# Performance work log

Hardware: AMD Instinct MI355X
Metric: run time of the kernel (lower is better)

Reference implementation:

```python
import jax, jax.numpy as jnp
import numpy as np

NEG = jnp.float32(-1e30)  # log-semiring 'zero' (avoid -inf for safe grads)


def _ctc_total_scores(log_probs, targets, input_lengths, target_lengths):
    """Log-semiring forward over the composed CTC topology.

    log_probs: (T, N, C) log-softmax outputs, blank id = 0
    targets:   (N*L,) flat labels in [1, C)
    Returns tot_scores (N,): log p(targets | log_probs) per utterance,
    identical to k2.intersect_dense + get_tot_scores(log_semiring=True).
    """
    T, N, C = log_probs.shape
    L = targets.shape[0] // N
    tgt = targets.reshape(N, L).astype(jnp.int32)
    S = 2 * L + 1  # extended sequence: blank y1 blank y2 ... yL blank

    ext = jnp.zeros((N, S), jnp.int32).at[:, 1::2].set(tgt)
    s_idx = jnp.arange(S)
    # skip transition s-2 -> s allowed only for label states with ext[s] != ext[s-2]
    diff = jnp.concatenate([jnp.zeros((N, 2), bool), ext[:, 2:] != ext[:, :-2]], axis=1)
    skip_ok = (s_idx[None, :] % 2 == 1) & (s_idx[None, :] >= 2) & diff
    # states beyond this utterance's extended length are invalid
    valid = s_idx[None, :] <= 2 * target_lengths.astype(jnp.int32)[:, None]
    s_end = 2 * target_lengths.astype(jnp.int32)  # index of final blank state

    def emit(lp):  # (N, C) -> (N, S): gather log-probs of extended labels
        return jnp.take_along_axis(lp, ext, axis=1)

    e0 = emit(log_probs[0])
    a0 = jnp.full((N, S), NEG).at[:, 0].set(e0[:, 0]).at[:, 1].set(e0[:, 1])
    a0 = jnp.where(valid, a0, NEG)

    def final_score(a):  # logsumexp over the two accepting states
        last = jnp.take_along_axis(a, s_end[:, None], axis=1)[:, 0]
        prev = jnp.take_along_axis(a, (s_end - 1)[:, None], axis=1)[:, 0]
        return jnp.logaddexp(last, prev)

    def step(a, lp):
        sh1 = jnp.concatenate([jnp.full((N, 1), NEG), a[:, :-1]], axis=1)
        sh2 = jnp.concatenate([jnp.full((N, 2), NEG), a[:, :-2]], axis=1)
        sh2 = jnp.where(skip_ok, sh2, NEG)
        a_new = jnp.logaddexp(jnp.logaddexp(a, sh1), sh2) + emit(lp)
        a_new = jnp.where(valid, a_new, NEG)
        return a_new, final_score(a_new)

    _, finals = jax.lax.scan(step, a0, log_probs[1:])  # finals: (T-1, N)
    finals = jnp.concatenate([final_score(a0)[None], finals], axis=0)  # (T, N)
    tot = jnp.take_along_axis(finals, (input_lengths.astype(jnp.int32) - 1)[None, :], axis=0)[0]
    return tot


def setup_inputs() -> dict:
    key = jax.random.key(0)
    k1, k2_ = jax.random.split(key)
    T, N, C, L = 1500, 32, 1024, 100
    log_probs = jax.nn.log_softmax(
        jax.random.normal(k1, (T, N, C), dtype=jnp.float32), axis=-1)
    targets = jax.random.randint(k2_, (N * L,), 1, C, dtype=jnp.int32)  # no blanks
    input_lengths = jnp.full((N,), T, dtype=jnp.int32)
    target_lengths = jnp.full((N,), L, dtype=jnp.int32)
    return {"log_probs": log_probs, "targets": targets,
            "input_lengths": input_lengths, "target_lengths": target_lengths}


def reference(log_probs, targets, input_lengths, target_lengths):
    tot = _ctc_total_scores(log_probs, targets, input_lengths, target_lengths)
    # drop -inf (failed) segments like get_tot_objf_and_num_frames, then negate sum
    finite = tot > jnp.float32(-1e29)
    return -jnp.sum(jnp.where(finite, tot, 0.0))
```

## Files before the change

### kernel.cpp

```cpp
#include <hip/hip_runtime.h>
#include <stdint.h>

#define NEGF  (-1e30f)
#define LOG2E 1.4426950408889634f
#define LN2F  0.6931471805599453f

__device__ __forceinline__ float fexp2(float x) {
#if __has_builtin(__builtin_amdgcn_exp2f)
    return __builtin_amdgcn_exp2f(x);
#else
    return exp2f(x);
#endif
}
__device__ __forceinline__ float flog2(float x) {
#if __has_builtin(__builtin_amdgcn_logf)
    return __builtin_amdgcn_logf(x);
#else
    return log2f(x);
#endif
}
__device__ __forceinline__ float lse2(float a, float b) {
    float m  = fmaxf(a, b);
    float mn = fminf(a, b);
    return m + flog2(1.0f + fexp2(mn - m));
}

__device__ __forceinline__ float dpp_shr1(float x, float fill) {
    int r = __builtin_amdgcn_update_dpp(__float_as_int(fill), __float_as_int(x),
                                        0x138, 0xf, 0xf, false);
    return __int_as_float(r);
}
__device__ __forceinline__ float dpp_shl1(float x, float fill) {
    int r = __builtin_amdgcn_update_dpp(__float_as_int(fill), __float_as_int(x),
                                        0x130, 0xf, 0xf, false);
    return __int_as_float(r);
}

#define RB  16
#define VMW "s_waitcnt vmcnt(44)"

__device__ __forceinline__ void stage_row_c(const float* src, float* dst)
{
    const int lane = threadIdx.x;
    const float* g = src + (lane << 2);
    __builtin_amdgcn_global_load_lds((const __attribute__((address_space(1))) void*)(g),
        (__attribute__((address_space(3))) void*)(dst), 16, 0, 0);
    __builtin_amdgcn_global_load_lds((const __attribute__((address_space(1))) void*)(g + 256),
        (__attribute__((address_space(3))) void*)(dst + 256), 16, 0, 0);
    __builtin_amdgcn_global_load_lds((const __attribute__((address_space(1))) void*)(g + 512),
        (__attribute__((address_space(3))) void*)(dst + 512), 16, 0, 0);
    __builtin_amdgcn_global_load_lds((const __attribute__((address_space(1))) void*)(g + 768),
        (__attribute__((address_space(3))) void*)(dst + 768), 16, 0, 0);
}

__device__ __forceinline__ void lds_read3(uint32_t sb, uint32_t o1, uint32_t o3,
                                          float& eb, float& e1, float& e3)
{
    asm volatile("s_mov_b32 m0, -1\n\t"
                 "ds_read_b32 %0, %3\n\t"
                 "ds_read_b32 %1, %4\n\t"
                 "ds_read_b32 %2, %5"
                 : "=&v"(eb), "=&v"(e1), "=&v"(e3)
                 : "v"(sb), "v"(sb + o1), "v"(sb + o3)
                 : "memory");
}
__device__ __forceinline__ void lds_read4(uint32_t sb, uint32_t o1, uint32_t o3, uint32_t o5,
                                          float& eb, float& e1, float& e3, float& e5)
{
    asm volatile("s_mov_b32 m0, -1\n\t"
                 "ds_read_b32 %0, %4\n\t"
                 "ds_read_b32 %1, %5\n\t"
                 "ds_read_b32 %2, %6\n\t"
                 "ds_read_b32 %3, %7"
                 : "=&v"(eb), "=&v"(e1), "=&v"(e3), "=&v"(e5)
                 : "v"(sb), "v"(sb + o1), "v"(sb + o3), "v"(sb + o5)
                 : "memory");
}

#define LGKM_WAIT3(c, x0, x1, x2) \
    asm volatile("s_waitcnt lgkmcnt(" #c ")" : "+v"(x0), "+v"(x1), "+v"(x2) :: "memory")
#define LGKM_WAIT4(c, x0, x1, x2, x3) \
    asm volatile("s_waitcnt lgkmcnt(" #c ")" : "+v"(x0), "+v"(x1), "+v"(x2), "+v"(x3) :: "memory")

#define RENORM_LANE(x0, x1, x2, x3, DPPC)                                     \
  do {                                                                        \
    float m_ = fmaxf(fmaxf(x0, x1), fmaxf(x2, x3));                           \
    int   ei_ = (__float_as_int(m_) >> 23) & 0xff;                            \
    bool  z_  = (m_ == 0.0f);                                                 \
    float sc_ = z_ ? 1.0f : ((ei_ != 0) ? __int_as_float((254 - ei_) << 23)   \
                                        : __int_as_float(253 << 23));         \
    int   d_  = z_ ? 0 : ((ei_ != 0) ? (ei_ - 127) : -126);                   \
    int   eu_ = esum + d_;                                                    \
    int   en_ = __builtin_amdgcn_update_dpp(eu_, eu_, (DPPC), 0xf, 0xf, false);\
    esum = z_ ? en_ : eu_;                          \
    x0 *= sc_; x1 *= sc_; x2 *= sc_; x3 *= sc_;                               \
    int   ep_ = __builtin_amdgcn_update_dpp(esum, esum, (DPPC), 0xf, 0xf, false);\
    int   ce_ = ep_ - esum;                                                   \
    ce_ = ce_ < -126 ? -126 : (ce_ > 126 ? 126 : ce_);                        \
    cross = __int_as_float((ce_ + 127) << 23);                                \
  } while (0)

__global__ __launch_bounds__(64, 1)
void ctc_scan(const float* __restrict__ lp, const int* __restrict__ tgt,
              const int* __restrict__ ilen, const int* __restrict__ tlen,
              float* __restrict__ wsA, float* __restrict__ wsB,
              int T, int N, int C, int L)
{
    __shared__ float ring[RB * 1024];

    const int  b      = blockIdx.x;
    const bool is_fwd = (b < N);
    const int  n      = is_fwd ? b : (b - N);
    const int  lane   = threadIdx.x;
    const int  len_t  = tlen[n];
    const int  len_in = ilen[n];
    const int  tm     = (len_in - 1) >> 1;
    const int  send   = 2 * len_t;

    const long tb = (long)n * L;
    auto getT = [&](int k) -> int {
        return (k >= 0 && k < len_t) ? tgt[tb + k] : 0;
    };
    const int lm1 = getT(2 * lane - 1);
    const int l1  = getT(2 * lane);
    const int l2  = getT(2 * lane + 1);
    const int l3  = getT(2 * lane + 2);
    const uint32_t o1 = (uint32_t)l1 << 2;
    const uint32_t o3 = (uint32_t)l2 << 2;
    const uint32_t o5 = (uint32_t)l3 << 2;
    const bool skip1 = (lane > 0) && (l1 != lm1);
    const bool skip3 = (l2 != l1);
    const bool skip5 = (l3 != l2);
    const int  s0 = 4 * lane;

    const long   rstride = (long)N * C;
    const float* row0    = lp + (long)n * C;
    const uint32_t ringb =
        (uint32_t)(uintptr_t)(const __attribute__((address_space(3))) void*)ring;

    int    esum  = 0;
    float  cross = 1.0f;
    double dsum  = 0.0;

    if (is_fwd) {
        float eb0 = row0[0];
        float e10 = row0[l1];
        asm volatile("s_waitcnt vmcnt(0)" : "+v"(eb0), "+v"(e10) :: "memory");
        dsum = (double)eb0;
        float a0 = (lane == 0) ? 1.0f : 0.0f;
        float a1 = (lane == 0 && 1 <= send) ? fexp2((e10 - eb0) * LOG2E) : 0.0f;
        float a2 = 0.0f, a3 = 0.0f;
        float p3 = 0.0f;

        const int nsteps = tm;
        const int lim    = len_in - 1;
        for (int j = 0; j < RB - 1; ++j) {
            int r = 1 + j; if (r > lim) r = lim;
            stage_row_c(row0 + (long)r * rstride, ring + (j << 10));
        }
        int rr = (16 > lim) ? lim : 16;
        const float* pstage = row0 + (long)rr * rstride;

        asm volatile(VMW ::: "memory");
        float rb0, r1_0, r3_0, rb1, r1_1, r3_1;
        float rb2, r1_2, r3_2, rb3, r1_3, r3_3;
        lds_read3(ringb,         o1, o3, rb0, r1_0, r3_0);
        lds_read3(ringb + 4096,  o1, o3, rb1, r1_1, r3_1);
        lds_read3(ringb + 8192,  o1, o3, rb2, r1_2, r3_2);
        lds_read3(ringb + 12288, o1, o3, rb3, r1_3, r3_3);

#define FSLOT(u, s)                                                            \
  do {                                                                         \
    stage_row_c(pstage, ring + ((((u) + 15) & 15) << 10));                     \
    { int adv = (rr < lim); rr += adv; pstage += adv ? rstride : 0; }          \
    asm volatile(VMW ::: "memory");                                            \
    LGKM_WAIT3(9, rb##s, r1_##s, r3_##s);                                      \
    float cb = rb##s, c1v = r1_##s, c3v = r3_##s;                              \
    lds_read3(ringb + ((((u) + 4) & 15) << 12), o1, o3, rb##s, r1_##s, r3_##s);\
    float rv1 = fexp2((c1v - cb) * LOG2E);                                     \
    float rv3 = fexp2((c3v - cb) * LOG2E);                                     \
    dsum += (double)cb;                                                        \
    float n0 = a0 + p3;                                                        \
    float n1 = (a1 + a0 + (skip1 ? p3 : 0.0f)) * rv1;                          \
    float n2 = a2 + a1;                                                        \
    float n3 = (a3 + a2 + (skip3 ? a1 : 0.0f)) * rv3;                          \
    a0 = n0; a1 = n1; a2 = n2; a3 = n3;                                        \
    p3 = dpp_shr1(a3, 0.0f) * cross;                                           \
  } while (0)

#define RENORM_F() do { RENORM_LANE(a0, a1, a2, a3, 0x138);                    \
                        p3 = dpp_shr1(a3, 0.0f) * cross; } while (0)

        int i = 0;
        while (i + 16 <= nsteps) {
            FSLOT(0,0);  FSLOT(1,1);  FSLOT(2,2);  FSLOT(3,3);
            FSLOT(4,0);  FSLOT(5,1);  FSLOT(6,2);  FSLOT(7,3);
            RENORM_F();
            FSLOT(8,0);  FSLOT(9,1);  FSLOT(10,2); FSLOT(11,3);
            FSLOT(12,0); FSLOT(13,1); FSLOT(14,2); FSLOT(15,3);
            RENORM_F();
            i += 16;
        }
        asm volatile("s_waitcnt vmcnt(0) lgkmcnt(0)"
                     :: "v"(rb0), "v"(r1_0), "v"(r3_0), "v"(rb1), "v"(r1_1), "v"(r3_1),
                        "v"(rb2), "v"(r1_2), "v"(r3_2), "v"(rb3), "v"(r1_3), "v"(r3_3)
                     : "memory");
        for (; i < nsteps; ++i) {
            float cb, c1v, c3v;
            lds_read3(ringb + (uint32_t)((i & 15) << 12), o1, o3, cb, c1v, c3v);
            LGKM_WAIT3(0, cb, c1v, c3v);
            float rv1 = fexp2((c1v - cb) * LOG2E);
            float rv3 = fexp2((c3v - cb) * LOG2E);
            dsum += (double)cb;
            float n0 = a0 + p3;
            float n1 = (a1 + a0 + (skip1 ? p3 : 0.0f)) * rv1;
            float n2 = a2 + a1;
            float n3 = (a3 + a2 + (skip3 ? a1 : 0.0f)) * rv3;
            a0 = n0; a1 = n1; a2 = n2; a3 = n3;
            p3 = dpp_shr1(a3, 0.0f) * cross;
            if ((i & 7) == 7) RENORM_F();
        }
        float S  = (float)(dsum * 1.4426950408889634);
        float fe = (float)esum;
        float w0 = fmaxf(flog2(a0) + fe + S, NEGF);
        float w1 = fmaxf(flog2(a1) + fe + S, NEGF);
        float w2 = fmaxf(flog2(a2) + fe + S, NEGF);
        float w3 = fmaxf(flog2(a3) + fe + S, NEGF);
        *((float4*)(wsA + (long)n * 256) + lane) = make_float4(w0, w1, w2, w3);
#undef FSLOT
#undef RENORM_F
    } else {
        float b0 = (s0     == send || s0     == send - 1) ? 1.0f : 0.0f;
        float b1 = (s0 + 1 == send || s0 + 1 == send - 1) ? 1.0f : 0.0f;
        float b2 = (s0 + 2 == send || s0 + 2 == send - 1) ? 1.0f : 0.0f;
        float b3 = (s0 + 3 == send || s0 + 3 == send - 1) ? 1.0f : 0.0f;
        float q0 = dpp_shl1(b0, 0.0f);
        float q1 = dpp_shl1(b1, 0.0f);

        const int nsteps = len_in - 1 - tm;
        for (int j = 0; j < RB - 1; ++j) {
            int r = len_in - 1 - j; if (r < 0) r = 0;
            stage_row_c(row0 + (long)r * rstride, ring + (j << 10));
        }
        int rr = len_in - 16; if (rr < 0) rr = 0;
        const float* pstage = row0 + (long)rr * rstride;

        asm volatile(VMW ::: "memory");
        float rb0, r1_0, r3_0, r5_0, rb1, r1_1, r3_1, r5_1;
        float rb2, r1_2, r3_2, r5_2, rb3, r1_3, r3_3, r5_3;
        lds_read4(ringb,         o1, o3, o5, rb0, r1_0, r3_0, r5_0);
        lds_read4(ringb + 4096,  o1, o3, o5, rb1, r1_1, r3_1, r5_1);
        lds_read4(ringb + 8192,  o1, o3, o5, rb2, r1_2, r3_2, r5_2);
        lds_read4(ringb + 12288, o1, o3, o5, rb3, r1_3, r3_3, r5_3);

#define BSLOT(u, s)                                                            \
  do {                                                                         \
    stage_row_c(pstage, ring + ((((u) + 15) & 15) << 10));                     \
    { int adv = (rr > 0); rr -= adv; pstage -= adv ? rstride : 0; }            \
    asm volatile(VMW ::: "memory");                                            \
    LGKM_WAIT4(12, rb##s, r1_##s, r3_##s, r5_##s);                             \
    float cb = rb##s, c1v = r1_##s, c3v = r3_##s, c5v = r5_##s;                \
    lds_read4(ringb + ((((u) + 4) & 15) << 12), o1, o3, o5,                    \
              rb##s, r1_##s, r3_##s, r5_##s);                                  \
    float rv1 = fexp2((c1v - cb) * LOG2E);                                     \
    float rv3 = fexp2((c3v - cb) * LOG2E);                                     \
    float rv5 = fexp2((c5v - cb) * LOG2E);                                     \
    dsum += (double)cb;                                                        \
    float g1 = b1 * rv1, g3 = b3 * rv3;                                        \
    float n0 = b0 + g1;                                                        \
    float n1 = g1 + b2 + (skip3 ? g3 : 0.0f);                                  \
    float n2 = b2 + g3;                                                        \
    float n3 = g3 + q0 + (skip5 ? q1 * rv5 : 0.0f);                            \
    b0 = n0; b1 = n1; b2 = n2; b3 = n3;                                        \
    q0 = dpp_shl1(b0, 0.0f) * cross;                                           \
    q1 = dpp_shl1(b1, 0.0f) * cross;                                           \
  } while (0)

#define RENORM_B() do { RENORM_LANE(b0, b1, b2, b3, 0x130);                    \
                        q0 = dpp_shl1(b0, 0.0f) * cross;                       \
                        q1 = dpp_shl1(b1, 0.0f) * cross; } while (0)

        int i = 0;
        while (i + 16 <= nsteps) {
            BSLOT(0,0);  BSLOT(1,1);  BSLOT(2,2);  BSLOT(3,3);
            BSLOT(4,0);  BSLOT(5,1);  BSLOT(6,2);  BSLOT(7,3);
            RENORM_B();
            BSLOT(8,0);  BSLOT(9,1);  BSLOT(10,2); BSLOT(11,3);
            BSLOT(12,0); BSLOT(13,1); BSLOT(14,2); BSLOT(15,3);
            RENORM_B();
            i += 16;
        }
        asm volatile("s_waitcnt vmcnt(0) lgkmcnt(0)"
                     :: "v"(rb0), "v"(r1_0), "v"(r3_0), "v"(r5_0),
                        "v"(rb1), "v"(r1_1), "v"(r3_1), "v"(r5_1),
                        "v"(rb2), "v"(r1_2), "v"(r3_2), "v"(r5_2),
                        "v"(rb3), "v"(r1_3), "v"(r3_3), "v"(r5_3)
                     : "memory");
        for (; i < nsteps; ++i) {
            float cb, c1v, c3v, c5v;
            lds_read4(ringb + (uint32_t)((i & 15) << 12), o1, o3, o5,
                      cb, c1v, c3v, c5v);
            LGKM_WAIT4(0, cb, c1v, c3v, c5v);
            float rv1 = fexp2((c1v - cb) * LOG2E);
            float rv3 = fexp2((c3v - cb) * LOG2E);
            float rv5 = fexp2((c5v - cb) * LOG2E);
            dsum += (double)cb;
            float g1 = b1 * rv1, g3 = b3 * rv3;
            float n0 = b0 + g1;
            float n1 = g1 + b2 + (skip3 ? g3 : 0.0f);
            float n2 = b2 + g3;
            float n3 = g3 + q0 + (skip5 ? q1 * rv5 : 0.0f);
            b0 = n0; b1 = n1; b2 = n2; b3 = n3;
            q0 = dpp_shl1(b0, 0.0f) * cross;
            q1 = dpp_shl1(b1, 0.0f) * cross;
            if ((i & 7) == 7) RENORM_B();
        }
        float S  = (float)(dsum * 1.4426950408889634);
        float fe = (float)esum;
        float w0 = fmaxf(flog2(b0) + fe + S, NEGF);
        float w1 = fmaxf(flog2(b1) + fe + S, NEGF);
        float w2 = fmaxf(flog2(b2) + fe + S, NEGF);
        float w3 = fmaxf(flog2(b3) + fe + S, NEGF);
        *((float4*)(wsB + (long)n * 256) + lane) = make_float4(w0, w1, w2, w3);
#undef BSLOT
#undef RENORM_B
    }
}

__global__ __launch_bounds__(64, 1)
void ctc_combine(const float* __restrict__ wsA, const float* __restrict__ wsB,
                 float* __restrict__ out)
{
    const int n = blockIdx.x;
    const int lane = threadIdx.x;
    const float4 A = *((const float4*)(wsA + (long)n * 256) + lane);
    const float4 B = *((const float4*)(wsB + (long)n * 256) + lane);
    float v = lse2(lse2(A.x + B.x, A.y + B.y), lse2(A.z + B.z, A.w + B.w));
    #pragma unroll
    for (int off = 1; off < 64; off <<= 1) {
        float o = __shfl_xor(v, off, 64);
        v = lse2(v, o);
    }
    if (lane == 0) {
        float tot = v * LN2F;
        if (tot > -1e29f) atomicAdd(out, -tot);
    }
}

extern "C" void kernel_launch(void* const* d_in, const int* in_sizes, int n_in,
                              void* d_out, int out_size, void* d_ws, size_t ws_size,
                              hipStream_t stream) {
    const float* lp      = (const float*)d_in[0];
    const int*   targets = (const int*)d_in[1];
    const int*   in_len  = (const int*)d_in[2];
    const int*   tgt_len = (const int*)d_in[3];
    const int N = in_sizes[2];
    const int L = in_sizes[1] / N;
    const int C = 1024;
    const int T = (int)((long)in_sizes[0] / ((long)N * C));

    float* out = (float*)d_out;
    float* wsA = (float*)d_ws;
    float* wsB = wsA + (long)N * 256;

    hipMemsetAsync(out, 0, sizeof(float), stream);
    ctc_scan<<<2 * N, 64, 0, stream>>>(lp, targets, in_len, tgt_len,
                                       wsA, wsB, T, N, C, L);
    ctc_combine<<<N, 64, 0, stream>>>(wsA, wsB, out);
}
```

Baseline: 319.9 us.

## Split row staging across four waves with barrier-synchronized 32-row LDS ring

```diff
diff --git a/kernel.cpp b/kernel.cpp
--- a/kernel.cpp
+++ b/kernel.cpp
@@ -36,22 +36,7 @@
     return __int_as_float(r);
 }
 
-#define RB  16
-#define VMW "s_waitcnt vmcnt(44)"
-
-__device__ __forceinline__ void stage_row_c(const float* src, float* dst)
-{
-    const int lane = threadIdx.x;
-    const float* g = src + (lane << 2);
-    __builtin_amdgcn_global_load_lds((const __attribute__((address_space(1))) void*)(g),
-        (__attribute__((address_space(3))) void*)(dst), 16, 0, 0);
-    __builtin_amdgcn_global_load_lds((const __attribute__((address_space(1))) void*)(g + 256),
-        (__attribute__((address_space(3))) void*)(dst + 256), 16, 0, 0);
-    __builtin_amdgcn_global_load_lds((const __attribute__((address_space(1))) void*)(g + 512),
-        (__attribute__((address_space(3))) void*)(dst + 512), 16, 0, 0);
-    __builtin_amdgcn_global_load_lds((const __attribute__((address_space(1))) void*)(g + 768),
-        (__attribute__((address_space(3))) void*)(dst + 768), 16, 0, 0);
-}
+#define VMW "s_waitcnt vmcnt(20)"
 
 __device__ __forceinline__ void lds_read3(uint32_t sb, uint32_t o1, uint32_t o3,
                                           float& eb, float& e1, float& e3)
@@ -100,22 +85,24 @@
     cross = __int_as_float((ce_ + 127) << 23);                                \
   } while (0)
 
-__global__ __launch_bounds__(64, 1)
+__global__ __launch_bounds__(256, 1)
 void ctc_scan(const float* __restrict__ lp, const int* __restrict__ tgt,
               const int* __restrict__ ilen, const int* __restrict__ tlen,
               float* __restrict__ wsA, float* __restrict__ wsB,
               int T, int N, int C, int L)
 {
-    __shared__ float ring[RB * 1024];
+    __shared__ float ring[32 * 1024];
 
     const int  b      = blockIdx.x;
     const bool is_fwd = (b < N);
     const int  n      = is_fwd ? b : (b - N);
-    const int  lane   = threadIdx.x;
+    const int  lane   = threadIdx.x & 63;
+    const int  wid    = threadIdx.x >> 6;
     const int  len_t  = tlen[n];
     const int  len_in = ilen[n];
     const int  tm     = (len_in - 1) >> 1;
     const int  send   = 2 * len_t;
+    const int  lim    = len_in - 1;
 
     const long tb = (long)n * L;
     auto getT = [&](int k) -> int {
@@ -135,196 +122,160 @@
 
     const long   rstride = (long)N * C;
     const float* row0    = lp + (long)n * C;
+    const int    qbase   = wid << 8;
     const uint32_t ringb =
         (uint32_t)(uintptr_t)(const __attribute__((address_space(3))) void*)ring;
+
+    const int nsteps  = is_fwd ? tm : (len_in - 1 - tm);
+    const int ngroups = nsteps >> 2;
+
+    auto stage_group = [&](int G) {
+        #pragma unroll
+        for (int j = 0; j < 4; ++j) {
+            int s = 4 * G + j;
+            long r = is_fwd ? (long)(1 + s) : (long)(len_in - 1 - s);
+            if (r > lim) r = lim;
+            if (r < 0)  r = 0;
+            const float* src = row0 + r * rstride + qbase + (lane << 2);
+            float*       dst = ring + ((s & 31) << 10) + qbase;
+            __builtin_amdgcn_global_load_lds(
+                (const __attribute__((address_space(1))) void*)src,
+                (__attribute__((address_space(3))) void*)dst, 16, 0, 0);
+        }
+    };
 
     int    esum  = 0;
     float  cross = 1.0f;
     double dsum  = 0.0;
 
+    float a0, a1, a2, a3, p3;
+    float b0, b1, b2, b3, q0, q1;
     if (is_fwd) {
         float eb0 = row0[0];
         float e10 = row0[l1];
         asm volatile("s_waitcnt vmcnt(0)" : "+v"(eb0), "+v"(e10) :: "memory");
         dsum = (double)eb0;
-        float a0 = (lane == 0) ? 1.0f : 0.0f;
-        float a1 = (lane == 0 && 1 <= send) ? fexp2((e10 - eb0) * LOG2E) : 0.0f;
-        float a2 = 0.0f, a3 = 0.0f;
-        float p3 = 0.0f;
-
-        const int nsteps = tm;
-        const int lim    = len_in - 1;
-        for (int j = 0; j < RB - 1; ++j) {
-            int r = 1 + j; if (r > lim) r = lim;
-            stage_row_c(row0 + (long)r * rstride, ring + (j << 10));
+        a0 = (lane == 0) ? 1.0f : 0.0f;
+        a1 = (lane == 0 && 1 <= send) ? fexp2((e10 - eb0) * LOG2E) : 0.0f;
+        a2 = 0.0f; a3 = 0.0f; p3 = 0.0f;
+    } else {
+        asm volatile("s_waitcnt vmcnt(0)" ::: "memory");
+        b0 = (s0     == send || s0     == send - 1) ? 1.0f : 0.0f;
+        b1 = (s0 + 1 == send || s0 + 1 == send - 1) ? 1.0f : 0.0f;
+        b2 = (s0 + 2 == send || s0 + 2 == send - 1) ? 1.0f : 0.0f;
+        b3 = (s0 + 3 == send || s0 + 3 == send - 1) ? 1.0f : 0.0f;
+        q0 = dpp_shl1(b0, 0.0f);
+        q1 = dpp_shl1(b1, 0.0f);
+    }
+
+    for (int G = 0; G < 6; ++G) stage_group(G);
+    asm volatile(VMW ::: "memory");
+
+    for (int g = 0; g < ngroups; ++g) {
+        stage_group(g + 6);
+        asm volatile(VMW ::: "memory");
+        __builtin_amdgcn_s_barrier();
+        if (wid == 0) {
+            uint32_t sb = ringb + (uint32_t)(((4 * g) & 31) << 12);
+            if (is_fwd) {
+                float cb0,c10,c30, cb1,c11,c31, cb2,c12,c32, cb3,c13,c33;
+                lds_read3(sb,         o1, o3, cb0, c10, c30);
+                lds_read3(sb + 4096,  o1, o3, cb1, c11, c31);
+                lds_read3(sb + 8192,  o1, o3, cb2, c12, c32);
+                lds_read3(sb + 12288, o1, o3, cb3, c13, c33);
+#define FSTEP(cb, c1v, c3v)                                                   \
+  do {                                                                        \
+    float rv1 = fexp2(((c1v) - (cb)) * LOG2E);                                \
+    float rv3 = fexp2(((c3v) - (cb)) * LOG2E);                                \
+    float n0 = a0 + p3;                                                       \
+    float n1 = (a1 + a0 + (skip1 ? p3 : 0.0f)) * rv1;                         \
+    float n2 = a2 + a1;                                                       \
+    float n3 = (a3 + a2 + (skip3 ? a1 : 0.0f)) * rv3;                         \
+    a0 = n0; a1 = n1; a2 = n2; a3 = n3;                                       \
+    p3 = dpp_shr1(a3, 0.0f) * cross;                                          \
+  } while (0)
+                LGKM_WAIT3(9, cb0, c10, c30); FSTEP(cb0, c10, c30);
+                LGKM_WAIT3(6, cb1, c11, c31); FSTEP(cb1, c11, c31);
+                LGKM_WAIT3(3, cb2, c12, c32); FSTEP(cb2, c12, c32);
+                LGKM_WAIT3(0, cb3, c13, c33); FSTEP(cb3, c13, c33);
+                dsum += (double)((cb0 + cb1) + (cb2 + cb3));
+                if (g & 1) {
+                    RENORM_LANE(a0, a1, a2, a3, 0x138);
+                    p3 = dpp_shr1(a3, 0.0f) * cross;
+                }
+            } else {
+                float cb0,c10,c30,c50, cb1,c11,c31,c51;
+                float cb2,c12,c32,c52, cb3,c13,c33,c53;
+                lds_read4(sb,         o1, o3, o5, cb0, c10, c30, c50);
+                lds_read4(sb + 4096,  o1, o3, o5, cb1, c11, c31, c51);
+                lds_read4(sb + 8192,  o1, o3, o5, cb2, c12, c32, c52);
+                lds_read4(sb + 12288, o1, o3, o5, cb3, c13, c33, c53);
+#define BSTEP(cb, c1v, c3v, c5v)                                              \
+  do {                                                                        \
+    float rv1 = fexp2(((c1v) - (cb)) * LOG2E);                                \
+    float rv3 = fexp2(((c3v) - (cb)) * LOG2E);                                \
+    float rv5 = fexp2(((c5v) - (cb)) * LOG2E);                                \
+    float g1 = b1 * rv1, g3 = b3 * rv3;                                       \
+    float n0 = b0 + g1;                                                       \
+    float n1 = g1 + b2 + (skip3 ? g3 : 0.0f);                                 \
+    float n2 = b2 + g3;                                                       \
+    float n3 = g3 + q0 + (skip5 ? q1 * rv5 : 0.0f);                           \
+    b0 = n0; b1 = n1; b2 = n2; b3 = n3;                                       \
+    q0 = dpp_shl1(b0, 0.0f) * cross;                                          \
+    q1 = dpp_shl1(b1, 0.0f) * cross;                                          \
+  } while (0)
+                LGKM_WAIT4(12, cb0, c10, c30, c50); BSTEP(cb0, c10, c30, c50);
+                LGKM_WAIT4(8,  cb1, c11, c31, c51); BSTEP(cb1, c11, c31, c51);
+                LGKM_WAIT4(4,  cb2, c12, c32, c52); BSTEP(cb2, c12, c32, c52);
+                LGKM_WAIT4(0,  cb3, c13, c33, c53); BSTEP(cb3, c13, c33, c53);
+                dsum += (double)((cb0 + cb1) + (cb2 + cb3));
+                if (g & 1) {
+                    RENORM_LANE(b0, b1, b2, b3, 0x130);
+                    q0 = dpp_shl1(b0, 0.0f) * cross;
+                    q1 = dpp_shl1(b1, 0.0f) * cross;
+                }
+            }
         }
-        int rr = (16 > lim) ? lim : 16;
-        const float* pstage = row0 + (long)rr * rstride;
-
-        asm volatile(VMW ::: "memory");
-        float rb0, r1_0, r3_0, rb1, r1_1, r3_1;
-        float rb2, r1_2, r3_2, rb3, r1_3, r3_3;
-        lds_read3(ringb,         o1, o3, rb0, r1_0, r3_0);
-        lds_read3(ringb + 4096,  o1, o3, rb1, r1_1, r3_1);
-        lds_read3(ringb + 8192,  o1, o3, rb2, r1_2, r3_2);
-        lds_read3(ringb + 12288, o1, o3, rb3, r1_3, r3_3);
-
-#define FSLOT(u, s)                                                            \
-  do {                                                                         \
-    stage_row_c(pstage, ring + ((((u) + 15) & 15) << 10));                     \
-    { int adv = (rr < lim); rr += adv; pstage += adv ? rstride : 0; }          \
-    asm volatile(VMW ::: "memory");                                            \
-    LGKM_WAIT3(9, rb##s, r1_##s, r3_##s);                                      \
-    float cb = rb##s, c1v = r1_##s, c3v = r3_##s;                              \
-    lds_read3(ringb + ((((u) + 4) & 15) << 12), o1, o3, rb##s, r1_##s, r3_##s);\
-    float rv1 = fexp2((c1v - cb) * LOG2E);                                     \
-    float rv3 = fexp2((c3v - cb) * LOG2E);                                     \
-    dsum += (double)cb;                                                        \
-    float n0 = a0 + p3;                                                        \
-    float n1 = (a1 + a0 + (skip1 ? p3 : 0.0f)) * rv1;                          \
-    float n2 = a2 + a1;                                                        \
-    float n3 = (a3 + a2 + (skip3 ? a1 : 0.0f)) * rv3;                          \
-    a0 = n0; a1 = n1; a2 = n2; a3 = n3;                                        \
-    p3 = dpp_shr1(a3, 0.0f) * cross;                                           \
-  } while (0)
-
-#define RENORM_F() do { RENORM_LANE(a0, a1, a2, a3, 0x138);                    \
-                        p3 = dpp_shr1(a3, 0.0f) * cross; } while (0)
-
-        int i = 0;
-        while (i + 16 <= nsteps) {
-            FSLOT(0,0);  FSLOT(1,1);  FSLOT(2,2);  FSLOT(3,3);
-            FSLOT(4,0);  FSLOT(5,1);  FSLOT(6,2);  FSLOT(7,3);
-            RENORM_F();
-            FSLOT(8,0);  FSLOT(9,1);  FSLOT(10,2); FSLOT(11,3);
-            FSLOT(12,0); FSLOT(13,1); FSLOT(14,2); FSLOT(15,3);
-            RENORM_F();
-            i += 16;
+    }
+
+    asm volatile("s_waitcnt vmcnt(0) lgkmcnt(0)" ::: "memory");
+    __builtin_amdgcn_s_barrier();
+    if (wid == 0) {
+        if (is_fwd) {
+            for (int i = 4 * ngroups; i < nsteps; ++i) {
+                float cb, c1v, c3v;
+                lds_read3(ringb + (uint32_t)((i & 31) << 12), o1, o3, cb, c1v, c3v);
+                LGKM_WAIT3(0, cb, c1v, c3v);
+                FSTEP(cb, c1v, c3v);
+                dsum += (double)cb;
+            }
+            float S  = (float)(dsum * 1.4426950408889634);
+            float fe = (float)esum;
+            float w0 = fmaxf(flog2(a0) + fe + S, NEGF);
+            float w1 = fmaxf(flog2(a1) + fe + S, NEGF);
+            float w2 = fmaxf(flog2(a2) + fe + S, NEGF);
+            float w3 = fmaxf(flog2(a3) + fe + S, NEGF);
+            *((float4*)(wsA + (long)n * 256) + lane) = make_float4(w0, w1, w2, w3);
+        } else {
+            for (int i = 4 * ngroups; i < nsteps; ++i) {
+                float cb, c1v, c3v, c5v;
+                lds_read4(ringb + (uint32_t)((i & 31) << 12), o1, o3, o5,
+                          cb, c1v, c3v, c5v);
+                LGKM_WAIT4(0, cb, c1v, c3v, c5v);
+                BSTEP(cb, c1v, c3v, c5v);
+                dsum += (double)cb;
+            }
+            float S  = (float)(dsum * 1.4426950408889634);
+            float fe = (float)esum;
+            float w0 = fmaxf(flog2(b0) + fe + S, NEGF);
+            float w1 = fmaxf(flog2(b1) + fe + S, NEGF);
+            float w2 = fmaxf(flog2(b2) + fe + S, NEGF);
+            float w3 = fmaxf(flog2(b3) + fe + S, NEGF);
+            *((float4*)(wsB + (long)n * 256) + lane) = make_float4(w0, w1, w2, w3);
         }
-        asm volatile("s_waitcnt vmcnt(0) lgkmcnt(0)"
-                     :: "v"(rb0), "v"(r1_0), "v"(r3_0), "v"(rb1), "v"(r1_1), "v"(r3_1),
-                        "v"(rb2), "v"(r1_2), "v"(r3_2), "v"(rb3), "v"(r1_3), "v"(r3_3)
-                     : "memory");
-        for (; i < nsteps; ++i) {
-            float cb, c1v, c3v;
-            lds_read3(ringb + (uint32_t)((i & 15) << 12), o1, o3, cb, c1v, c3v);
-            LGKM_WAIT3(0, cb, c1v, c3v);
-            float rv1 = fexp2((c1v - cb) * LOG2E);
-            float rv3 = fexp2((c3v - cb) * LOG2E);
-            dsum += (double)cb;
-            float n0 = a0 + p3;
-            float n1 = (a1 + a0 + (skip1 ? p3 : 0.0f)) * rv1;
-            float n2 = a2 + a1;
-            float n3 = (a3 + a2 + (skip3 ? a1 : 0.0f)) * rv3;
-            a0 = n0; a1 = n1; a2 = n2; a3 = n3;
-            p3 = dpp_shr1(a3, 0.0f) * cross;
-            if ((i & 7) == 7) RENORM_F();
-        }
-        float S  = (float)(dsum * 1.4426950408889634);
-        float fe = (float)esum;
-        float w0 = fmaxf(flog2(a0) + fe + S, NEGF);
-        float w1 = fmaxf(flog2(a1) + fe + S, NEGF);
-        float w2 = fmaxf(flog2(a2) + fe + S, NEGF);
-        float w3 = fmaxf(flog2(a3) + fe + S, NEGF);
-        *((float4*)(wsA + (long)n * 256) + lane) = make_float4(w0, w1, w2, w3);
-#undef FSLOT
-#undef RENORM_F
-    } else {
-        float b0 = (s0     == send || s0     == send - 1) ? 1.0f : 0.0f;
-        float b1 = (s0 + 1 == send || s0 + 1 == send - 1) ? 1.0f : 0.0f;
-        float b2 = (s0 + 2 == send || s0 + 2 == send - 1) ? 1.0f : 0.0f;
-        float b3 = (s0 + 3 == send || s0 + 3 == send - 1) ? 1.0f : 0.0f;
-        float q0 = dpp_shl1(b0, 0.0f);
-        float q1 = dpp_shl1(b1, 0.0f);
-
-        const int nsteps = len_in - 1 - tm;
-        for (int j = 0; j < RB - 1; ++j) {
-            int r = len_in - 1 - j; if (r < 0) r = 0;
-            stage_row_c(row0 + (long)r * rstride, ring + (j << 10));
-        }
-        int rr = len_in - 16; if (rr < 0) rr = 0;
-        const float* pstage = row0 + (long)rr * rstride;
-
-        asm volatile(VMW ::: "memory");
-        float rb0, r1_0, r3_0, r5_0, rb1, r1_1, r3_1, r5_1;
-        float rb2, r1_2, r3_2, r5_2, rb3, r1_3, r3_3, r5_3;
-        lds_read4(ringb,         o1, o3, o5, rb0, r1_0, r3_0, r5_0);
-        lds_read4(ringb + 4096,  o1, o3, o5, rb1, r1_1, r3_1, r5_1);
-        lds_read4(ringb + 8192,  o1, o3, o5, rb2, r1_2, r3_2, r5_2);
-        lds_read4(ringb + 12288, o1, o3, o5, rb3, r1_3, r3_3, r5_3);
-
-#define BSLOT(u, s)                                                            \
-  do {                                                                         \
-    stage_row_c(pstage, ring + ((((u) + 15) & 15) << 10));                     \
-    { int adv = (rr > 0); rr -= adv; pstage -= adv ? rstride : 0; }            \
-    asm volatile(VMW ::: "memory");                                            \
-    LGKM_WAIT4(12, rb##s, r1_##s, r3_##s, r5_##s);                             \
-    float cb = rb##s, c1v = r1_##s, c3v = r3_##s, c5v = r5_##s;                \
-    lds_read4(ringb + ((((u) + 4) & 15) << 12), o1, o3, o5,                    \
-              rb##s, r1_##s, r3_##s, r5_##s);                                  \
-    float rv1 = fexp2((c1v - cb) * LOG2E);                                     \
-    float rv3 = fexp2((c3v - cb) * LOG2E);                                     \
-    float rv5 = fexp2((c5v - cb) * LOG2E);                                     \
-    dsum += (double)cb;                                                        \
-    float g1 = b1 * rv1, g3 = b3 * rv3;                                        \
-    float n0 = b0 + g1;                                                        \
-    float n1 = g1 + b2 + (skip3 ? g3 : 0.0f);                                  \
-    float n2 = b2 + g3;                                                        \
-    float n3 = g3 + q0 + (skip5 ? q1 * rv5 : 0.0f);                            \
-    b0 = n0; b1 = n1; b2 = n2; b3 = n3;                                        \
-    q0 = dpp_shl1(b0, 0.0f) * cross;                                           \
-    q1 = dpp_shl1(b1, 0.0f) * cross;                                           \
-  } while (0)
-
-#define RENORM_B() do { RENORM_LANE(b0, b1, b2, b3, 0x130);                    \
-                        q0 = dpp_shl1(b0, 0.0f) * cross;                       \
-                        q1 = dpp_shl1(b1, 0.0f) * cross; } while (0)
-
-        int i = 0;
-        while (i + 16 <= nsteps) {
-            BSLOT(0,0);  BSLOT(1,1);  BSLOT(2,2);  BSLOT(3,3);
-            BSLOT(4,0);  BSLOT(5,1);  BSLOT(6,2);  BSLOT(7,3);
-            RENORM_B();
-            BSLOT(8,0);  BSLOT(9,1);  BSLOT(10,2); BSLOT(11,3);
-            BSLOT(12,0); BSLOT(13,1); BSLOT(14,2); BSLOT(15,3);
-            RENORM_B();
-            i += 16;
-        }
-        asm volatile("s_waitcnt vmcnt(0) lgkmcnt(0)"
-                     :: "v"(rb0), "v"(r1_0), "v"(r3_0), "v"(r5_0),
-                        "v"(rb1), "v"(r1_1), "v"(r3_1), "v"(r5_1),
-                        "v"(rb2), "v"(r1_2), "v"(r3_2), "v"(r5_2),
-                        "v"(rb3), "v"(r1_3), "v"(r3_3), "v"(r5_3)
-                     : "memory");
-        for (; i < nsteps; ++i) {
-            float cb, c1v, c3v, c5v;
-            lds_read4(ringb + (uint32_t)((i & 15) << 12), o1, o3, o5,
-                      cb, c1v, c3v, c5v);
-            LGKM_WAIT4(0, cb, c1v, c3v, c5v);
-            float rv1 = fexp2((c1v - cb) * LOG2E);
-            float rv3 = fexp2((c3v - cb) * LOG2E);
-            float rv5 = fexp2((c5v - cb) * LOG2E);
-            dsum += (double)cb;
-            float g1 = b1 * rv1, g3 = b3 * rv3;
-            float n0 = b0 + g1;
-            float n1 = g1 + b2 + (skip3 ? g3 : 0.0f);
-            float n2 = b2 + g3;
-            float n3 = g3 + q0 + (skip5 ? q1 * rv5 : 0.0f);
-            b0 = n0; b1 = n1; b2 = n2; b3 = n3;
-            q0 = dpp_shl1(b0, 0.0f) * cross;
-            q1 = dpp_shl1(b1, 0.0f) * cross;
-            if ((i & 7) == 7) RENORM_B();
-        }
-        float S  = (float)(dsum * 1.4426950408889634);
-        float fe = (float)esum;
-        float w0 = fmaxf(flog2(b0) + fe + S, NEGF);
-        float w1 = fmaxf(flog2(b1) + fe + S, NEGF);
-        float w2 = fmaxf(flog2(b2) + fe + S, NEGF);
-        float w3 = fmaxf(flog2(b3) + fe + S, NEGF);
-        *((float4*)(wsB + (long)n * 256) + lane) = make_float4(w0, w1, w2, w3);
-#undef BSLOT
-#undef RENORM_B
-    }
+    }
+#undef FSTEP
+#undef BSTEP
 }
 
 __global__ __launch_bounds__(64, 1)
@@ -364,7 +315,7 @@
     float* wsB = wsA + (long)N * 256;
 
     hipMemsetAsync(out, 0, sizeof(float), stream);
-    ctc_scan<<<2 * N, 64, 0, stream>>>(lp, targets, in_len, tgt_len,
-                                       wsA, wsB, T, N, C, L);
+    ctc_scan<<<2 * N, 256, 0, stream>>>(lp, targets, in_len, tgt_len,
+                                        wsA, wsB, T, N, C, L);
     ctc_combine<<<N, 64, 0, stream>>>(wsA, wsB, out);
 }
```

After: 312.2 us. 1.02x faster.

## Pre-gather target log-probs into compact buffer before serial CTC scan

Applied to the files above, without the earlier changes.

```diff
diff --git a/kernel.cpp b/kernel.cpp
--- a/kernel.cpp
+++ b/kernel.cpp
@@ -36,8 +36,7 @@
     return __int_as_float(r);
 }
 
-#define RB  16
-#define VMW "s_waitcnt vmcnt(44)"
+#define VMW "s_waitcnt vmcnt(11)"
 
 __device__ __forceinline__ void stage_row_c(const float* src, float* dst)
 {
@@ -45,12 +44,6 @@
     const float* g = src + (lane << 2);
     __builtin_amdgcn_global_load_lds((const __attribute__((address_space(1))) void*)(g),
         (__attribute__((address_space(3))) void*)(dst), 16, 0, 0);
-    __builtin_amdgcn_global_load_lds((const __attribute__((address_space(1))) void*)(g + 256),
-        (__attribute__((address_space(3))) void*)(dst + 256), 16, 0, 0);
-    __builtin_amdgcn_global_load_lds((const __attribute__((address_space(1))) void*)(g + 512),
-        (__attribute__((address_space(3))) void*)(dst + 512), 16, 0, 0);
-    __builtin_amdgcn_global_load_lds((const __attribute__((address_space(1))) void*)(g + 768),
-        (__attribute__((address_space(3))) void*)(dst + 768), 16, 0, 0);
 }
 
 __device__ __forceinline__ void lds_read3(uint32_t sb, uint32_t o1, uint32_t o3,
@@ -100,13 +93,41 @@
     cross = __int_as_float((ce_ + 127) << 23);                                \
   } while (0)
 
+__global__ __launch_bounds__(128)
+void ctc_gather(const float* __restrict__ lp, const int* __restrict__ tgt,
+                const int* __restrict__ tlen, float* __restrict__ cbuf,
+                int T, int N, int C, int L)
+{
+    const int TILES = (T + 31) >> 5;
+    const int nb    = blockIdx.x / TILES;
+    const int tile  = blockIdx.x % TILES;
+    const int tid   = threadIdx.x;
+    const int len_t = tlen[nb];
+    const int idx   = (tid < len_t && tid < L) ? tgt[(long)nb * L + tid] : 0;
+    int t0 = tile << 5, t1 = t0 + 32; if (t1 > T) t1 = T;
+    const long  NC = (long)N * C;
+    const float* p = lp + (long)nb * C;
+    float*      cb = cbuf + (long)nb * T * 256;
+    for (int t = t0; t < t1; ++t) {
+        float v = p[(long)t * NC + idx];
+        float* crow = cb + ((long)t << 8);
+        crow[1 + tid] = v;
+        if (tid == 0) {
+            float bl = p[(long)t * NC];
+            crow[0]   = bl;
+            crow[129] = bl;
+        }
+    }
+}
+
 __global__ __launch_bounds__(64, 1)
-void ctc_scan(const float* __restrict__ lp, const int* __restrict__ tgt,
-              const int* __restrict__ ilen, const int* __restrict__ tlen,
+void ctc_scan(const float* __restrict__ lp, const float* __restrict__ cbuf,
+              const int* __restrict__ tgt, const int* __restrict__ ilen,
+              const int* __restrict__ tlen,
               float* __restrict__ wsA, float* __restrict__ wsB,
               int T, int N, int C, int L)
 {
-    __shared__ float ring[RB * 1024];
+    __shared__ float ring[16 * 256];
 
     const int  b      = blockIdx.x;
     const bool is_fwd = (b < N);
@@ -125,16 +146,16 @@
     const int l1  = getT(2 * lane);
     const int l2  = getT(2 * lane + 1);
     const int l3  = getT(2 * lane + 2);
-    const uint32_t o1 = (uint32_t)l1 << 2;
-    const uint32_t o3 = (uint32_t)l2 << 2;
-    const uint32_t o5 = (uint32_t)l3 << 2;
+    const uint32_t o1 = ((uint32_t)lane << 3) + 4;
+    const uint32_t o3 = o1 + 4;
+    const uint32_t o5 = o1 + 8;
     const bool skip1 = (lane > 0) && (l1 != lm1);
     const bool skip3 = (l2 != l1);
     const bool skip5 = (l3 != l2);
     const int  s0 = 4 * lane;
 
-    const long   rstride = (long)N * C;
     const float* row0    = lp + (long)n * C;
+    const float* crow0   = cbuf + (long)n * T * 256;
     const uint32_t ringb =
         (uint32_t)(uintptr_t)(const __attribute__((address_space(3))) void*)ring;
 
@@ -154,29 +175,29 @@
 
         const int nsteps = tm;
         const int lim    = len_in - 1;
-        for (int j = 0; j < RB - 1; ++j) {
+        for (int j = 0; j < 15; ++j) {
             int r = 1 + j; if (r > lim) r = lim;
-            stage_row_c(row0 + (long)r * rstride, ring + (j << 10));
+            stage_row_c(crow0 + ((long)r << 8), ring + (j << 8));
         }
         int rr = (16 > lim) ? lim : 16;
-        const float* pstage = row0 + (long)rr * rstride;
+        const float* pstage = crow0 + ((long)rr << 8);
 
         asm volatile(VMW ::: "memory");
         float rb0, r1_0, r3_0, rb1, r1_1, r3_1;
         float rb2, r1_2, r3_2, rb3, r1_3, r3_3;
-        lds_read3(ringb,         o1, o3, rb0, r1_0, r3_0);
-        lds_read3(ringb + 4096,  o1, o3, rb1, r1_1, r3_1);
-        lds_read3(ringb + 8192,  o1, o3, rb2, r1_2, r3_2);
-        lds_read3(ringb + 12288, o1, o3, rb3, r1_3, r3_3);
+        lds_read3(ringb,        o1, o3, rb0, r1_0, r3_0);
+        lds_read3(ringb + 1024, o1, o3, rb1, r1_1, r3_1);
+        lds_read3(ringb + 2048, o1, o3, rb2, r1_2, r3_2);
+        lds_read3(ringb + 3072, o1, o3, rb3, r1_3, r3_3);
 
 #define FSLOT(u, s)                                                            \
   do {                                                                         \
-    stage_row_c(pstage, ring + ((((u) + 15) & 15) << 10));                     \
-    { int adv = (rr < lim); rr += adv; pstage += adv ? rstride : 0; }          \
+    stage_row_c(pstage, ring + ((((u) + 15) & 15) << 8));                      \
+    { int adv = (rr < lim); rr += adv; pstage += adv ? 256 : 0; }              \
     asm volatile(VMW ::: "memory");                                            \
     LGKM_WAIT3(9, rb##s, r1_##s, r3_##s);                                      \
     float cb = rb##s, c1v = r1_##s, c3v = r3_##s;                              \
-    lds_read3(ringb + ((((u) + 4) & 15) << 12), o1, o3, rb##s, r1_##s, r3_##s);\
+    lds_read3(ringb + ((((u) + 4) & 15) << 10), o1, o3, rb##s, r1_##s, r3_##s);\
     float rv1 = fexp2((c1v - cb) * LOG2E);                                     \
     float rv3 = fexp2((c3v - cb) * LOG2E);                                     \
     dsum += (double)cb;                                                        \
@@ -207,7 +228,7 @@
                      : "memory");
         for (; i < nsteps; ++i) {
             float cb, c1v, c3v;
-            lds_read3(ringb + (uint32_t)((i & 15) << 12), o1, o3, cb, c1v, c3v);
+            lds_read3(ringb + (uint32_t)((i & 15) << 10), o1, o3, cb, c1v, c3v);
             LGKM_WAIT3(0, cb, c1v, c3v);
             float rv1 = fexp2((c1v - cb) * LOG2E);
             float rv3 = fexp2((c3v - cb) * LOG2E);
@@ -238,29 +259,29 @@
         float q1 = dpp_shl1(b1, 0.0f);
 
         const int nsteps = len_in - 1 - tm;
-        for (int j = 0; j < RB - 1; ++j) {
+        for (int j = 0; j < 15; ++j) {
             int r = len_in - 1 - j; if (r < 0) r = 0;
-            stage_row_c(row0 + (long)r * rstride, ring + (j << 10));
+            stage_row_c(crow0 + ((long)r << 8), ring + (j << 8));
         }
         int rr = len_in - 16; if (rr < 0) rr = 0;
-        const float* pstage = row0 + (long)rr * rstride;
+        const float* pstage = crow0 + ((long)rr << 8);
 
         asm volatile(VMW ::: "memory");
         float rb0, r1_0, r3_0, r5_0, rb1, r1_1, r3_1, r5_1;
         float rb2, r1_2, r3_2, r5_2, rb3, r1_3, r3_3, r5_3;
-        lds_read4(ringb,         o1, o3, o5, rb0, r1_0, r3_0, r5_0);
-        lds_read4(ringb + 4096,  o1, o3, o5, rb1, r1_1, r3_1, r5_1);
-        lds_read4(ringb + 8192,  o1, o3, o5, rb2, r1_2, r3_2, r5_2);
-        lds_read4(ringb + 12288, o1, o3, o5, rb3, r1_3, r3_3, r5_3);
+        lds_read4(ringb,        o1, o3, o5, rb0, r1_0, r3_0, r5_0);
+        lds_read4(ringb + 1024, o1, o3, o5, rb1, r1_1, r3_1, r5_1);
+        lds_read4(ringb + 2048, o1, o3, o5, rb2, r1_2, r3_2, r5_2);
+        lds_read4(ringb + 3072, o1, o3, o5, rb3, r1_3, r3_3, r5_3);
 
 #define BSLOT(u, s)                                                            \
   do {                                                                         \
-    stage_row_c(pstage, ring + ((((u) + 15) & 15) << 10));                     \
-    { int adv = (rr > 0); rr -= adv; pstage -= adv ? rstride : 0; }            \
+    stage_row_c(pstage, ring + ((((u) + 15) & 15) << 8));                      \
+    { int adv = (rr > 0); rr -= adv; pstage -= adv ? 256 : 0; }                \
     asm volatile(VMW ::: "memory");                                            \
     LGKM_WAIT4(12, rb##s, r1_##s, r3_##s, r5_##s);                             \
     float cb = rb##s, c1v = r1_##s, c3v = r3_##s, c5v = r5_##s;                \
-    lds_read4(ringb + ((((u) + 4) & 15) << 12), o1, o3, o5,                    \
+    lds_read4(ringb + ((((u) + 4) & 15) << 10), o1, o3, o5,                    \
               rb##s, r1_##s, r3_##s, r5_##s);                                  \
     float rv1 = fexp2((c1v - cb) * LOG2E);                                     \
     float rv3 = fexp2((c3v - cb) * LOG2E);                                     \
@@ -298,7 +319,7 @@
                      : "memory");
         for (; i < nsteps; ++i) {
             float cb, c1v, c3v, c5v;
-            lds_read4(ringb + (uint32_t)((i & 15) << 12), o1, o3, o5,
+            lds_read4(ringb + (uint32_t)((i & 15) << 10), o1, o3, o5,
                       cb, c1v, c3v, c5v);
             LGKM_WAIT4(0, cb, c1v, c3v, c5v);
             float rv1 = fexp2((c1v - cb) * LOG2E);
@@ -359,12 +380,17 @@
     const int C = 1024;
     const int T = (int)((long)in_sizes[0] / ((long)N * C));
 
-    float* out = (float*)d_out;
-    float* wsA = (float*)d_ws;
-    float* wsB = wsA + (long)N * 256;
+    float* out  = (float*)d_out;
+    float* wsA  = (float*)d_ws;
+    float* wsB  = wsA + (long)N * 256;
+    float* cbuf = wsB + (long)N * 256;
+
+    const int TILES = (T + 31) >> 5;
 
     hipMemsetAsync(out, 0, sizeof(float), stream);
-    ctc_scan<<<2 * N, 64, 0, stream>>>(lp, targets, in_len, tgt_len,
+    ctc_gather<<<N * TILES, 128, 0, stream>>>(lp, targets, tgt_len, cbuf,
+                                              T, N, C, L);
+    ctc_scan<<<2 * N, 64, 0, stream>>>(lp, cbuf, targets, in_len, tgt_len,
                                        wsA, wsB, T, N, C, L);
     ctc_combine<<<N, 64, 0, stream>>>(wsA, wsB, out);
 }
```

New measurement: 358.8 us. 12.1% more time.
